# Performance work log

Hardware: AMD Instinct MI355X
Metric: run time of the kernel (lower is better)

Reference implementation:

```python
import jax, jax.numpy as jnp
import numpy as np

B, N, NPOINT, NSAMPLE = 16, 4096, 1024, 32
RADIUS = 0.4
MLP = [64, 64, 128]
IN_CH = 6
EPS = 1e-5


def setup_inputs() -> dict:
    key = jax.random.key(0)
    ks = jax.random.split(key, 2 + 2 * len(MLP))
    inp = {
        "xyz": jax.random.normal(ks[0], (B, 3, N), jnp.float32),
        "points": jax.random.normal(ks[1], (B, 3, N), jnp.float32),
    }
    c_in = IN_CH
    for i, c_out in enumerate(MLP):
        inp[f"W{i}"] = jax.random.normal(ks[2 + 2 * i], (c_out, c_in), jnp.float32) / np.sqrt(c_in).astype(np.float32)
        inp[f"b{i}"] = jnp.zeros((c_out,), jnp.float32)
        inp[f"g{i}"] = jnp.ones((c_out,), jnp.float32)
        inp[f"beta{i}"] = jnp.zeros((c_out,), jnp.float32)
        c_in = c_out
    return inp


def _gather(points, idx):
    # points: [B, N, C], idx: [B, ...] int -> [B, ..., C]
    Bv = points.shape[0]
    flat = idx.reshape(Bv, -1)
    out = jnp.take_along_axis(points, flat[..., None], axis=1)
    return out.reshape(idx.shape + (points.shape[-1],))


def _fps(xyz, npoint):
    # xyz: [B, N, 3] -> centroid indices [B, npoint]
    Bv, Nv, _ = xyz.shape
    bidx = jnp.arange(Bv)

    def step(carry, _):
        dist, far = carry
        cen = xyz[bidx, far][:, None, :]                 # [B,1,3]
        d = jnp.sum((xyz - cen) ** 2, axis=-1)           # [B,N]
        dist = jnp.minimum(dist, d)
        return (dist, jnp.argmax(dist, axis=-1)), far

    init = (jnp.full((Bv, Nv), 1e10, xyz.dtype), jnp.zeros((Bv,), jnp.int32))
    _, cents = jax.lax.scan(step, init, None, length=npoint)
    return jnp.transpose(cents)                          # [B, npoint]


def _square_distance(src, dst):
    # src [B,S,3], dst [B,N,3] -> [B,S,N]
    return (jnp.sum(src ** 2, -1)[:, :, None]
            + jnp.sum(dst ** 2, -1)[:, None, :]
            - 2.0 * jnp.einsum('bsc,bnc->bsn', src, dst))


def _ball_query(radius, nsample, xyz, new_xyz):
    Nv = xyz.shape[1]
    sqr = _square_distance(new_xyz, xyz)                 # [B,S,N]
    arange = jnp.arange(Nv, dtype=jnp.int32)[None, None, :]
    idx = jnp.where(sqr > radius ** 2, Nv, arange)       # invalid -> sentinel N
    idx = jnp.sort(idx, axis=-1)[:, :, :nsample]         # [B,S,K]
    first = idx[:, :, :1]
    return jnp.where(idx == Nv, first, idx)


def reference(xyz, points, W0, b0, g0, beta0, W1, b1, g1, beta1, W2, b2, g2, beta2):
    xyz_t = jnp.transpose(xyz, (0, 2, 1))                # [B,N,3]
    pts_t = jnp.transpose(points, (0, 2, 1))             # [B,N,D]

    fps_idx = _fps(xyz_t, NPOINT)                        # [B,S]
    new_xyz = _gather(xyz_t, fps_idx)                    # [B,S,3]
    idx = _ball_query(RADIUS, NSAMPLE, xyz_t, new_xyz)   # [B,S,K]

    g_xyz = _gather(xyz_t, idx) - new_xyz[:, :, None, :] # [B,S,K,3]
    g_pts = _gather(pts_t, idx)                          # [B,S,K,D]
    feats = jnp.concatenate([g_xyz, g_pts], axis=-1)     # [B,S,K,C]

    for W, b, g, be in ((W0, b0, g0, beta0), (W1, b1, g1, beta1), (W2, b2, g2, beta2)):
        feats = jnp.einsum('bskc,oc->bsko', feats, W) + b
        mean = feats.mean(axis=(0, 1, 2))                # BN train mode stats
        var = feats.var(axis=(0, 1, 2))
        feats = g * (feats - mean) * jax.lax.rsqrt(var + EPS) + be
        feats = jax.nn.relu(feats)

    out = feats.max(axis=2)                              # max over nsample -> [B,S,C]
    return jnp.transpose(new_xyz, (0, 2, 1)), jnp.transpose(out, (0, 2, 1))
```

## Files before the change

### kernel.cpp

```cpp
#include <hip/hip_runtime.h>
#include <hip/hip_bf16.h>

#define B_ 16
#define N_ 4096
#define S_ 1024
#define K_ 32
#define R_ (B_*S_*K_)
#define NBLK_ (R_/64)

typedef unsigned short u16;
typedef __attribute__((ext_vector_type(8))) short bf16x8;
typedef __attribute__((ext_vector_type(4))) float f32x4;

__device__ __forceinline__ u16 f2bf(float f) {
    __hip_bfloat16 h = __float2bfloat16(f);
    return __builtin_bit_cast(u16, h);
}
__device__ __forceinline__ float bf2f(u16 u) {
    unsigned x = ((unsigned)u) << 16;
    return __builtin_bit_cast(float, x);
}

template <int CTRL>
__device__ __forceinline__ double dpp_max_f64(double v) {
    unsigned long long b = (unsigned long long)__double_as_longlong(v);
    int lo = (int)(unsigned)b;
    int hi = (int)(unsigned)(b >> 32);
    int olo = __builtin_amdgcn_update_dpp(lo, lo, CTRL, 0xF, 0xF, false);
    int ohi = __builtin_amdgcn_update_dpp(hi, hi, CTRL, 0xF, 0xF, false);
    double o = __longlong_as_double(
        (long long)(((unsigned long long)(unsigned)ohi << 32) | (unsigned)olo));
    return fmax(v, o);
}

__device__ __forceinline__ double packd(double d, int idx) {
    unsigned long long b = (unsigned long long)__double_as_longlong(d);
    b = (b & ~0xFFFull) | (unsigned)idx;
    return __longlong_as_double((long long)b);
}

__global__ __launch_bounds__(512, 2) void fps_kernel(const float* __restrict__ xyz,
                                                     float* __restrict__ out0) {
    const int b = blockIdx.x;
    const int tid = threadIdx.x;
    const int lane = tid & 63, wid = tid >> 6;
    __shared__ float4 p4[N_];
    __shared__ double candd[2][8];
    const float* xb = xyz + (size_t)b * 3 * N_;

    double x64[8], y64[8], z64[8], q64[8], dist[8];
#pragma unroll
    for (int j = 0; j < 8; ++j) {
        int i = tid + j * 512;
        float x = xb[i], y = xb[N_ + i], z = xb[2 * N_ + i];
        p4[i] = make_float4(x, y, z, 0.f);
        x64[j] = (double)x; y64[j] = (double)y; z64[j] = (double)z;
        q64[j] = x64[j] * x64[j] + y64[j] * y64[j] + z64[j] * z64[j];
        dist[j] = 1e30;
    }
    __syncthreads();

    int far = 0;
    int f0 = 0, f1 = 0;
    for (int s = 0; s < 1023; ++s) {
        float4 c = p4[far];
        f0 = (tid == s) ? far : f0;
        f1 = (tid + 512 == s) ? far : f1;
        double cx = (double)c.x, cy = (double)c.y, cz = (double)c.z;
        double c2p = cx * cx + cy * cy + cz * cz + 1.0;
        double A = -2.0 * cx, Bc = -2.0 * cy, Cc = -2.0 * cz;
#pragma unroll
        for (int j = 0; j < 8; ++j) {
            double d = fma(A, x64[j], fma(Bc, y64[j], fma(Cc, z64[j], q64[j] + c2p)));
            dist[j] = fmin(dist[j], packd(d, tid | (j << 9)));
        }
        double k = fmax(fmax(fmax(dist[0], dist[1]), fmax(dist[2], dist[3])),
                        fmax(fmax(dist[4], dist[5]), fmax(dist[6], dist[7])));
        k = dpp_max_f64<0x111>(k);
        k = dpp_max_f64<0x112>(k);
        k = dpp_max_f64<0x114>(k);
        k = dpp_max_f64<0x118>(k);
        k = dpp_max_f64<0x142>(k);
        k = dpp_max_f64<0x143>(k);
        int buf = s & 1;
        if (lane == 63) candd[buf][wid] = k;
        __syncthreads();
        double k2 = candd[buf][lane & 7];
        k2 = dpp_max_f64<0xB1>(k2);
        k2 = dpp_max_f64<0x4E>(k2);
        k2 = dpp_max_f64<0x124>(k2);
        unsigned lo = (unsigned)(unsigned long long)__double_as_longlong(k2);
        far = (int)(__builtin_amdgcn_readfirstlane(lo) & 0xFFFu);
    }
    if (tid == 511) f1 = far;
    {
        float4 c0 = p4[f0];
        out0[(size_t)b * 3072 + tid]        = c0.x;
        out0[(size_t)b * 3072 + 1024 + tid] = c0.y;
        out0[(size_t)b * 3072 + 2048 + tid] = c0.z;
        float4 c1 = p4[f1];
        out0[(size_t)b * 3072 + 512 + tid]        = c1.x;
        out0[(size_t)b * 3072 + 1024 + 512 + tid] = c1.y;
        out0[(size_t)b * 3072 + 2048 + 512 + tid] = c1.z;
    }
}

__global__ __launch_bounds__(256) void prep_kernel(const float* __restrict__ xyz,
                                                   const float* __restrict__ W1,
                                                   const float* __restrict__ W2,
                                                   u16* __restrict__ W1bf,
                                                   u16* __restrict__ W2bf,
                                                   double4* __restrict__ xyzq) {
    int t = blockIdx.x * 256 + threadIdx.x;
    if (t < 4096) W1bf[t] = f2bf(W1[t]);
    if (t < 8192) W2bf[t] = f2bf(W2[t]);
    int b = t >> 12, i = t & 4095;
    const float* xb = xyz + (size_t)b * 3 * N_;
    double x = (double)xb[i], y = (double)xb[N_ + i], z = (double)xb[2 * N_ + i];
    double4 v; v.x = x; v.y = y; v.z = z; v.w = x * x + y * y + z * z;
    xyzq[t] = v;
}

__global__ __launch_bounds__(256) void ballq_kernel(const double4* __restrict__ xyzq,
                                                    const float* __restrict__ out0,
                                                    int* __restrict__ idxbuf) {
    int wid = threadIdx.x >> 6, lane = threadIdx.x & 63;
    int m = blockIdx.x * 4 + wid;
    int b = m >> 10, s = m & 1023;
    const double4* pb = xyzq + (size_t)b * N_;
    double cx = (double)out0[b * 3072 + s];
    double cy = (double)out0[b * 3072 + 1024 + s];
    double cz = (double)out0[b * 3072 + 2048 + s];
    double c2 = cx * cx + cy * cy + cz * cz;
    const double rr = 0.4 * 0.4;
    int* ob = idxbuf + (size_t)m * K_;
    int cnt = 0, first = -1;
    for (int ch = 0; ch < N_ / 64; ++ch) {
        int i = ch * 64 + lane;
        double4 p = pb[i];
        double dot = cx * p.x + cy * p.y + cz * p.z;
        double sqr = (c2 + p.w) - 2.0 * dot;
        bool in = !(sqr > rr);
        unsigned long long mask = __ballot(in);
        if (in) {
            int pos = cnt + __popcll(mask & ((1ull << lane) - 1ull));
            if (pos < K_) ob[pos] = i;
        }
        if (cnt == 0 && mask) first = ch * 64 + (__ffsll((long long)mask) - 1);
        cnt += __popcll(mask);
        if (cnt >= K_) break;
    }
    if (cnt < K_ && lane >= cnt && lane < K_) ob[lane] = first;
}

__global__ __launch_bounds__(256) void gather_stats0(
        const float* __restrict__ xyz, const float* __restrict__ pts,
        const float* __restrict__ out0, const int* __restrict__ idxbuf,
        const float* __restrict__ W0, const float* __restrict__ b0,
        float* __restrict__ F, float2* __restrict__ part) {
    __shared__ float Fs[64][6];
    __shared__ float W0s[384];
    __shared__ float b0s[64];
    __shared__ float2 red[4][64];
    int tid = threadIdx.x;
    long rowbase = (long)blockIdx.x * 64;
    for (int e = tid; e < 384; e += 256) {
        int r = e / 6, c = e - r * 6;
        long rw = rowbase + r;
        int b = (int)(rw >> 15);
        int s = ((int)(rw & 32767)) >> 5;
        int i = idxbuf[rw];
        float v;
        if (c < 3)
            v = xyz[(size_t)b * 3 * N_ + c * N_ + i] - out0[b * 3072 + c * 1024 + s];
        else
            v = pts[(size_t)b * 3 * N_ + (c - 3) * N_ + i];
        Fs[r][c] = v;
        F[rw * 6 + c] = v;
    }
    if (tid < 64) b0s[tid] = b0[tid];
    for (int t = tid; t < 384; t += 256) W0s[t] = W0[t];
    __syncthreads();
    int o = tid & 63, rg = tid >> 6;
    float w[6];
#pragma unroll
    for (int c = 0; c < 6; ++c) w[c] = W0s[o * 6 + c];
    float sum = 0.f, sq = 0.f;
#pragma unroll
    for (int rr = 0; rr < 16; ++rr) {
        int rl = rg * 16 + rr;
        float y = b0s[o];
#pragma unroll
        for (int c = 0; c < 6; ++c) y += Fs[rl][c] * w[c];
        sum += y; sq += y * y;
    }
    red[rg][o] = make_float2(sum, sq);
    __syncthreads();
    if (tid < 64) {
        float2 t0 = red[0][tid], t1 = red[1][tid], t2 = red[2][tid], t3 = red[3][tid];
        part[(size_t)blockIdx.x * 64 + tid] =
            make_float2(t0.x + t1.x + t2.x + t3.x, t0.y + t1.y + t2.y + t3.y);
    }
}

__global__ __launch_bounds__(256) void reduce_stats(const float2* __restrict__ part,
                                                    int nblk, int C,
                                                    const float* __restrict__ g,
                                                    const float* __restrict__ beta,
                                                    float* __restrict__ scale,
                                                    float* __restrict__ shift) {
    int o = blockIdx.x;
    int tid = threadIdx.x;
    double s = 0.0, q = 0.0;
    for (int i = tid; i < nblk; i += 256) {
        float2 v = part[(size_t)i * C + o];
        s += (double)v.x; q += (double)v.y;
    }
    __shared__ double ss[256], qq[256];
    ss[tid] = s; qq[tid] = q;
    __syncthreads();
    for (int m = 128; m > 0; m >>= 1) {
        if (tid < m) { ss[tid] += ss[tid + m]; qq[tid] += qq[tid + m]; }
        __syncthreads();
    }
    if (tid == 0) {
        const double Rd = (double)R_;
        double mean = ss[0] / Rd;
        double var = qq[0] / Rd - mean * mean;
        double sc = (double)g[o] / sqrt(var + 1e-5);
        scale[o] = (float)sc;
        shift[o] = (float)((double)beta[o] - mean * sc);
    }
}

__global__ __launch_bounds__(256) void layer1_mfma(
        const float* __restrict__ F, const float* __restrict__ W0,
        const float* __restrict__ b0, const float* __restrict__ scale0,
        const float* __restrict__ shift0, const u16* __restrict__ W1bf,
        const float* __restrict__ b1, u16* __restrict__ Y1bf,
        float2* __restrict__ part) {
    __shared__ float Fs[64][6];
    __shared__ float W0s[384];
    __shared__ float b0s[64], sc0[64], sh0[64];
    __shared__ u16 Xs[64][72];
    __shared__ float ssum[16][64];
    __shared__ float ssq[16][64];
    int tid = threadIdx.x;
    long rowbase = (long)blockIdx.x * 64;
    for (int t = tid; t < 384; t += 256) { Fs[t / 6][t % 6] = F[rowbase * 6 + t]; W0s[t] = W0[t]; }
    if (tid < 64) { b0s[tid] = b0[tid]; sc0[tid] = scale0[tid]; sh0[tid] = shift0[tid]; }
    __syncthreads();
    {
        int o = tid & 63, rg = tid >> 6;
        float w[6];
#pragma unroll
        for (int c = 0; c < 6; ++c) w[c] = W0s[o * 6 + c];
        float sc = sc0[o], sh = sh0[o], bb = b0s[o];
#pragma unroll
        for (int rr = 0; rr < 16; ++rr) {
            int rl = rg * 16 + rr;
            float y = bb;
#pragma unroll
            for (int c = 0; c < 6; ++c) y += Fs[rl][c] * w[c];
            Xs[rl][o] = f2bf(fmaxf(sc * y + sh, 0.f));
        }
    }
    __syncthreads();
    int l = tid & 63, w = tid >> 6;
    int ar = l & 15, kg = l >> 4;
    bf16x8 a0 = *(const bf16x8*)&Xs[w * 16 + ar][kg * 8];
    bf16x8 a1 = *(const bf16x8*)&Xs[w * 16 + ar][32 + kg * 8];
    f32x4 acc[4];
#pragma unroll
    for (int t4 = 0; t4 < 4; ++t4) acc[t4] = (f32x4){0.f, 0.f, 0.f, 0.f};
#pragma unroll
    for (int t4 = 0; t4 < 4; ++t4) {
        const u16* wp = &W1bf[(t4 * 16 + ar) * 64 + kg * 8];
        bf16x8 bfr0 = *(const bf16x8*)wp;
        bf16x8 bfr1 = *(const bf16x8*)(wp + 32);
        acc[t4] = __builtin_amdgcn_mfma_f32_16x16x32_bf16(a0, bfr0, acc[t4], 0, 0, 0);
        acc[t4] = __builtin_amdgcn_mfma_f32_16x16x32_bf16(a1, bfr1, acc[t4], 0, 0, 0);
    }
#pragma unroll
    for (int t4 = 0; t4 < 4; ++t4) {
        int col = t4 * 16 + ar;
        float bb = b1[col];
        float s = 0.f, q = 0.f;
#pragma unroll
        for (int r = 0; r < 4; ++r) {
            float y = acc[t4][r] + bb;
            int row = w * 16 + kg * 4 + r;
            Y1bf[(rowbase + row) * 64 + col] = f2bf(y);
            s += y; q += y * y;
        }
        ssum[w * 4 + kg][col] = s;
        ssq[w * 4 + kg][col] = q;
    }
    __syncthreads();
    if (tid < 64) {
        float s = 0.f, q = 0.f;
#pragma unroll
        for (int i = 0; i < 16; ++i) { s += ssum[i][tid]; q += ssq[i][tid]; }
        part[(size_t)blockIdx.x * 64 + tid] = make_float2(s, q);
    }
}

__global__ __launch_bounds__(256) void layer2_mfma(
        const u16* __restrict__ Y1bf, const float* __restrict__ scale1,
        const float* __restrict__ shift1, const u16* __restrict__ W2bf,
        const float* __restrict__ b2, float* __restrict__ gmax,
        float* __restrict__ gmin, float2* __restrict__ part) {
    __shared__ u16 Xs[64][72];
    __shared__ float sc1s[64], sh1s[64];
    __shared__ float mxs[16][128], mns[16][128];
    __shared__ float ssum[16][128], ssq[16][128];
    int tid = threadIdx.x;
    long rowbase = (long)blockIdx.x * 64;
    if (tid < 64) { sc1s[tid] = scale1[tid]; sh1s[tid] = shift1[tid]; }
    __syncthreads();
    {
        int r = tid >> 2, seg = (tid & 3) * 16;
        const u16* yp = &Y1bf[(rowbase + r) * 64 + seg];
        bf16x8 v0 = *(const bf16x8*)yp;
        bf16x8 v1 = *(const bf16x8*)(yp + 8);
#pragma unroll
        for (int j = 0; j < 8; ++j) {
            float x0 = fmaxf(sc1s[seg + j] * bf2f((u16)v0[j]) + sh1s[seg + j], 0.f);
            float x1 = fmaxf(sc1s[seg + 8 + j] * bf2f((u16)v1[j]) + sh1s[seg + 8 + j], 0.f);
            Xs[r][seg + j] = f2bf(x0);
            Xs[r][seg + 8 + j] = f2bf(x1);
        }
    }
    __syncthreads();
    int l = tid & 63, w = tid >> 6;
    int ar = l & 15, kg = l >> 4;
    bf16x8 a0 = *(const bf16x8*)&Xs[w * 16 + ar][kg * 8];
    bf16x8 a1 = *(const bf16x8*)&Xs[w * 16 + ar][32 + kg * 8];
    f32x4 acc[8];
#pragma unroll
    for (int t8 = 0; t8 < 8; ++t8) acc[t8] = (f32x4){0.f, 0.f, 0.f, 0.f};
#pragma unroll
    for (int t8 = 0; t8 < 8; ++t8) {
        const u16* wp = &W2bf[(t8 * 16 + ar) * 64 + kg * 8];
        bf16x8 bfr0 = *(const bf16x8*)wp;
        bf16x8 bfr1 = *(const bf16x8*)(wp + 32);
        acc[t8] = __builtin_amdgcn_mfma_f32_16x16x32_bf16(a0, bfr0, acc[t8], 0, 0, 0);
        acc[t8] = __builtin_amdgcn_mfma_f32_16x16x32_bf16(a1, bfr1, acc[t8], 0, 0, 0);
    }
#pragma unroll
    for (int t8 = 0; t8 < 8; ++t8) {
        int col = t8 * 16 + ar;
        float bb = b2[col];
        float y0 = acc[t8][0] + bb, y1 = acc[t8][1] + bb;
        float y2 = acc[t8][2] + bb, y3 = acc[t8][3] + bb;
        ssum[w * 4 + kg][col] = y0 + y1 + y2 + y3;
        ssq[w * 4 + kg][col] = y0 * y0 + y1 * y1 + y2 * y2 + y3 * y3;
        mxs[w * 4 + kg][col] = fmaxf(fmaxf(y0, y1), fmaxf(y2, y3));
        mns[w * 4 + kg][col] = fminf(fminf(y0, y1), fminf(y2, y3));
    }
    __syncthreads();
    if (tid < 128) {
        int col = tid;
        float s = 0.f, q = 0.f;
        float m0 = -3.0e38f, m1 = -3.0e38f, n0 = 3.0e38f, n1 = 3.0e38f;
#pragma unroll
        for (int i = 0; i < 8; ++i) {
            s += ssum[i][col]; q += ssq[i][col];
            m0 = fmaxf(m0, mxs[i][col]); n0 = fminf(n0, mns[i][col]);
        }
#pragma unroll
        for (int i = 8; i < 16; ++i) {
            s += ssum[i][col]; q += ssq[i][col];
            m1 = fmaxf(m1, mxs[i][col]); n1 = fminf(n1, mns[i][col]);
        }
        part[(size_t)blockIdx.x * 128 + col] = make_float2(s, q);
        gmax[((size_t)blockIdx.x * 2 + 0) * 128 + col] = m0;
        gmax[((size_t)blockIdx.x * 2 + 1) * 128 + col] = m1;
        gmin[((size_t)blockIdx.x * 2 + 0) * 128 + col] = n0;
        gmin[((size_t)blockIdx.x * 2 + 1) * 128 + col] = n1;
    }
}

__global__ __launch_bounds__(256) void final_kernel(const float* __restrict__ gmax,
                                                    const float* __restrict__ gmin,
                                                    const float* __restrict__ scale2,
                                                    const float* __restrict__ shift2,
                                                    float* __restrict__ out1) {
    int b = blockIdx.x, st = blockIdx.y, ot = blockIdx.z;
    __shared__ float tile[32][33];
    int tid = threadIdx.x;
    for (int e = tid; e < 1024; e += 256) {
        int sl = e >> 5, ol = e & 31;
        int s = st * 32 + sl, o = ot * 32 + ol;
        size_t m = (size_t)b * 1024 + s;
        float sc = scale2[o];
        float v = (sc >= 0.f) ? gmax[m * 128 + o] : gmin[m * 128 + o];
        tile[sl][ol] = fmaxf(sc * v + shift2[o], 0.f);
    }
    __syncthreads();
    for (int e = tid; e < 1024; e += 256) {
        int ol = e >> 5, sl = e & 31;
        int s = st * 32 + sl, o = ot * 32 + ol;
        out1[(size_t)b * 131072 + (size_t)o * 1024 + s] = tile[sl][ol];
    }
}

extern "C" void kernel_launch(void* const* d_in, const int* in_sizes, int n_in,
                              void* d_out, int out_size, void* d_ws, size_t ws_size,
                              hipStream_t stream) {
    const float* xyz   = (const float*)d_in[0];
    const float* pts   = (const float*)d_in[1];
    const float* W0    = (const float*)d_in[2];
    const float* b0    = (const float*)d_in[3];
    const float* g0    = (const float*)d_in[4];
    const float* beta0 = (const float*)d_in[5];
    const float* W1    = (const float*)d_in[6];
    const float* b1    = (const float*)d_in[7];
    const float* g1    = (const float*)d_in[8];
    const float* beta1 = (const float*)d_in[9];
    const float* W2    = (const float*)d_in[10];
    const float* b2    = (const float*)d_in[11];
    const float* g2    = (const float*)d_in[12];
    const float* beta2 = (const float*)d_in[13];

    float* out0 = (float*)d_out;
    float* out1 = (float*)d_out + 49152;

    char* w = (char*)d_ws;
    size_t off = 0;
    double4* xyzq = (double4*)(w + off);  off += (size_t)B_ * N_ * 32;
    int*    idxbuf = (int*)(w + off);    off += (size_t)R_ * 4;
    float*  F      = (float*)(w + off);  off += (size_t)R_ * 6 * 4;
    u16*    Y1bf   = (u16*)(w + off);    off += (size_t)R_ * 64 * 2;
    float*  gmax   = (float*)(w + off);  off += (size_t)B_ * S_ * 128 * 4;
    float*  gmin   = (float*)(w + off);  off += (size_t)B_ * S_ * 128 * 4;
    float2* part   = (float2*)(w + off); off += (size_t)NBLK_ * 128 * 2 * 4;
    u16*    W1bf   = (u16*)(w + off);    off += 4096 * 2;
    u16*    W2bf   = (u16*)(w + off);    off += 8192 * 2;
    float*  ss     = (float*)(w + off);  off += 512 * 4;
    float* scale0 = ss,       *shift0 = ss + 64;
    float* scale1 = ss + 128, *shift1 = ss + 192;
    float* scale2 = ss + 256, *shift2 = ss + 384;

    prep_kernel<<<256, 256, 0, stream>>>(xyz, W1, W2, W1bf, W2bf, xyzq);
    fps_kernel<<<B_, 512, 0, stream>>>(xyz, out0);
    ballq_kernel<<<(B_ * S_) / 4, 256, 0, stream>>>(xyzq, out0, idxbuf);
    gather_stats0<<<NBLK_, 256, 0, stream>>>(xyz, pts, out0, idxbuf, W0, b0, F, part);
    reduce_stats<<<64, 256, 0, stream>>>(part, NBLK_, 64, g0, beta0, scale0, shift0);
    layer1_mfma<<<NBLK_, 256, 0, stream>>>(F, W0, b0, scale0, shift0, W1bf, b1, Y1bf, part);
    reduce_stats<<<64, 256, 0, stream>>>(part, NBLK_, 64, g1, beta1, scale1, shift1);
    layer2_mfma<<<NBLK_, 256, 0, stream>>>(Y1bf, scale1, shift1, W2bf, b2, gmax, gmin, part);
    reduce_stats<<<128, 256, 0, stream>>>(part, NBLK_, 128, g2, beta2, scale2, shift2);
    final_kernel<<<dim3(B_, 32, 4), 256, 0, stream>>>(gmax, gmin, scale2, shift2, out1);
}
```

Measured before the change: 864.5 us.

## Fuse gather into ball query and derive layer-0 BN stats from input moments

The ball-query kernel now also gathers the grouped features and writes F. It accumulates the 6 first moments and 21 second moments of the inputs per block. Layer-0 batch-norm mean and variance come analytically from these moments and W0/b0 in double precision, which removes the separate gather_stats0 pass and the 64-channel reduction. The FPS kernel also caches precomputed -2x and |x|^2+1 doubles in shared memory to drop per-step centroid arithmetic, at the cost of more LDS and one block per CU. The moment-based variance is more prone to cancellation, and the per-block moments are summed in fp32.

```diff
diff --git a/kernel.cpp b/kernel.cpp
--- a/kernel.cpp
+++ b/kernel.cpp
@@ -39,12 +39,12 @@
     return __longlong_as_double((long long)b);
 }
 
-__global__ __launch_bounds__(512, 2) void fps_kernel(const float* __restrict__ xyz,
+__global__ __launch_bounds__(512, 1) void fps_kernel(const float* __restrict__ xyz,
                                                      float* __restrict__ out0) {
     const int b = blockIdx.x;
     const int tid = threadIdx.x;
     const int lane = tid & 63, wid = tid >> 6;
-    __shared__ float4 p4[N_];
+    __shared__ double4 cd[N_];
     __shared__ double candd[2][8];
     const float* xb = xyz + (size_t)b * 3 * N_;
 
@@ -53,9 +53,11 @@
     for (int j = 0; j < 8; ++j) {
         int i = tid + j * 512;
         float x = xb[i], y = xb[N_ + i], z = xb[2 * N_ + i];
-        p4[i] = make_float4(x, y, z, 0.f);
-        x64[j] = (double)x; y64[j] = (double)y; z64[j] = (double)z;
-        q64[j] = x64[j] * x64[j] + y64[j] * y64[j] + z64[j] * z64[j];
+        double dx = (double)x, dy = (double)y, dz = (double)z;
+        double q = dx * dx + dy * dy + dz * dz;
+        double4 v; v.x = -2.0 * dx; v.y = -2.0 * dy; v.z = -2.0 * dz; v.w = q + 1.0;
+        cd[i] = v;
+        x64[j] = dx; y64[j] = dy; z64[j] = dz; q64[j] = q;
         dist[j] = 1e30;
     }
     __syncthreads();
@@ -63,15 +65,12 @@
     int far = 0;
     int f0 = 0, f1 = 0;
     for (int s = 0; s < 1023; ++s) {
-        float4 c = p4[far];
+        double4 C = cd[far];
         f0 = (tid == s) ? far : f0;
         f1 = (tid + 512 == s) ? far : f1;
-        double cx = (double)c.x, cy = (double)c.y, cz = (double)c.z;
-        double c2p = cx * cx + cy * cy + cz * cz + 1.0;
-        double A = -2.0 * cx, Bc = -2.0 * cy, Cc = -2.0 * cz;
 #pragma unroll
         for (int j = 0; j < 8; ++j) {
-            double d = fma(A, x64[j], fma(Bc, y64[j], fma(Cc, z64[j], q64[j] + c2p)));
+            double d = fma(C.x, x64[j], fma(C.y, y64[j], fma(C.z, z64[j], q64[j] + C.w)));
             dist[j] = fmin(dist[j], packd(d, tid | (j << 9)));
         }
         double k = fmax(fmax(fmax(dist[0], dist[1]), fmax(dist[2], dist[3])),
@@ -94,14 +93,14 @@
     }
     if (tid == 511) f1 = far;
     {
-        float4 c0 = p4[f0];
-        out0[(size_t)b * 3072 + tid]        = c0.x;
-        out0[(size_t)b * 3072 + 1024 + tid] = c0.y;
-        out0[(size_t)b * 3072 + 2048 + tid] = c0.z;
-        float4 c1 = p4[f1];
-        out0[(size_t)b * 3072 + 512 + tid]        = c1.x;
-        out0[(size_t)b * 3072 + 1024 + 512 + tid] = c1.y;
-        out0[(size_t)b * 3072 + 2048 + 512 + tid] = c1.z;
+        double4 c0 = cd[f0];
+        out0[(size_t)b * 3072 + tid]        = (float)(-0.5 * c0.x);
+        out0[(size_t)b * 3072 + 1024 + tid] = (float)(-0.5 * c0.y);
+        out0[(size_t)b * 3072 + 2048 + tid] = (float)(-0.5 * c0.z);
+        double4 c1 = cd[f1];
+        out0[(size_t)b * 3072 + 512 + tid]        = (float)(-0.5 * c1.x);
+        out0[(size_t)b * 3072 + 1024 + 512 + tid] = (float)(-0.5 * c1.y);
+        out0[(size_t)b * 3072 + 2048 + 512 + tid] = (float)(-0.5 * c1.z);
     }
 }
 
@@ -121,9 +120,14 @@
     xyzq[t] = v;
 }
 
-__global__ __launch_bounds__(256) void ballq_kernel(const double4* __restrict__ xyzq,
-                                                    const float* __restrict__ out0,
-                                                    int* __restrict__ idxbuf) {
+__global__ __launch_bounds__(256) void ballq_gather(
+        const double4* __restrict__ xyzq, const float* __restrict__ out0,
+        const float* __restrict__ xyz, const float* __restrict__ pts,
+        int* __restrict__ idxbuf, float* __restrict__ F,
+        float* __restrict__ part0) {
+    __shared__ int idxs[4][32];
+    __shared__ float Ftile[128][6];
+    __shared__ float red[8][27];
     int wid = threadIdx.x >> 6, lane = threadIdx.x & 63;
     int m = blockIdx.x * 4 + wid;
     int b = m >> 10, s = m & 1023;
@@ -144,63 +148,99 @@
         unsigned long long mask = __ballot(in);
         if (in) {
             int pos = cnt + __popcll(mask & ((1ull << lane) - 1ull));
-            if (pos < K_) ob[pos] = i;
+            if (pos < K_) { ob[pos] = i; idxs[wid][pos] = i; }
         }
         if (cnt == 0 && mask) first = ch * 64 + (__ffsll((long long)mask) - 1);
         cnt += __popcll(mask);
         if (cnt >= K_) break;
     }
-    if (cnt < K_ && lane >= cnt && lane < K_) ob[lane] = first;
-}
-
-__global__ __launch_bounds__(256) void gather_stats0(
-        const float* __restrict__ xyz, const float* __restrict__ pts,
-        const float* __restrict__ out0, const int* __restrict__ idxbuf,
-        const float* __restrict__ W0, const float* __restrict__ b0,
-        float* __restrict__ F, float2* __restrict__ part) {
-    __shared__ float Fs[64][6];
-    __shared__ float W0s[384];
-    __shared__ float b0s[64];
-    __shared__ float2 red[4][64];
+    if (cnt < K_ && lane >= cnt && lane < K_) { ob[lane] = first; idxs[wid][lane] = first; }
+    __syncthreads();
+    if (lane < 32) {
+        int i = idxs[wid][lane];
+        int rl = wid * 32 + lane;
+        long rw = (long)m * 32 + lane;
+        float cxf = out0[b * 3072 + s], cyf = out0[b * 3072 + 1024 + s], czf = out0[b * 3072 + 2048 + s];
+        const float* xb = xyz + (size_t)b * 3 * N_;
+        const float* pp = pts + (size_t)b * 3 * N_;
+        float f0v = xb[i] - cxf, f1v = xb[N_ + i] - cyf, f2v = xb[2 * N_ + i] - czf;
+        float f3v = pp[i], f4v = pp[N_ + i], f5v = pp[2 * N_ + i];
+        Ftile[rl][0] = f0v; Ftile[rl][1] = f1v; Ftile[rl][2] = f2v;
+        Ftile[rl][3] = f3v; Ftile[rl][4] = f4v; Ftile[rl][5] = f5v;
+        float* Fg = F + rw * 6;
+        Fg[0] = f0v; Fg[1] = f1v; Fg[2] = f2v; Fg[3] = f3v; Fg[4] = f4v; Fg[5] = f5v;
+    }
+    __syncthreads();
+    int t = threadIdx.x;
+    if (t < 216) {
+        const int c1t[27] = {0,1,2,3,4,5, 0,0,0,0,0,0, 1,1,1,1,1, 2,2,2,2, 3,3,3, 4,4, 5};
+        const int c2t[27] = {0,1,2,3,4,5, 0,1,2,3,4,5, 1,2,3,4,5, 2,3,4,5, 3,4,5, 4,5, 5};
+        int st = t % 27, g = t / 27;
+        float acc = 0.f;
+        if (st < 6) {
+            for (int r = g * 16; r < g * 16 + 16; ++r) acc += Ftile[r][st];
+        } else {
+            int a = c1t[st], c = c2t[st];
+            for (int r = g * 16; r < g * 16 + 16; ++r) acc += Ftile[r][a] * Ftile[r][c];
+        }
+        red[g][st] = acc;
+    }
+    __syncthreads();
+    if (t < 27) {
+        float a = 0.f;
+#pragma unroll
+        for (int g = 0; g < 8; ++g) a += red[g][t];
+        part0[(size_t)blockIdx.x * 27 + t] = a;
+    }
+}
+
+__global__ __launch_bounds__(256) void reduce27(const float* __restrict__ part0,
+                                                double* __restrict__ G) {
+    int st = blockIdx.x;
     int tid = threadIdx.x;
-    long rowbase = (long)blockIdx.x * 64;
-    for (int e = tid; e < 384; e += 256) {
-        int r = e / 6, c = e - r * 6;
-        long rw = rowbase + r;
-        int b = (int)(rw >> 15);
-        int s = ((int)(rw & 32767)) >> 5;
-        int i = idxbuf[rw];
-        float v;
-        if (c < 3)
-            v = xyz[(size_t)b * 3 * N_ + c * N_ + i] - out0[b * 3072 + c * 1024 + s];
-        else
-            v = pts[(size_t)b * 3 * N_ + (c - 3) * N_ + i];
-        Fs[r][c] = v;
-        F[rw * 6 + c] = v;
-    }
-    if (tid < 64) b0s[tid] = b0[tid];
-    for (int t = tid; t < 384; t += 256) W0s[t] = W0[t];
-    __syncthreads();
-    int o = tid & 63, rg = tid >> 6;
-    float w[6];
-#pragma unroll
-    for (int c = 0; c < 6; ++c) w[c] = W0s[o * 6 + c];
-    float sum = 0.f, sq = 0.f;
-#pragma unroll
-    for (int rr = 0; rr < 16; ++rr) {
-        int rl = rg * 16 + rr;
-        float y = b0s[o];
-#pragma unroll
-        for (int c = 0; c < 6; ++c) y += Fs[rl][c] * w[c];
-        sum += y; sq += y * y;
-    }
-    red[rg][o] = make_float2(sum, sq);
-    __syncthreads();
-    if (tid < 64) {
-        float2 t0 = red[0][tid], t1 = red[1][tid], t2 = red[2][tid], t3 = red[3][tid];
-        part[(size_t)blockIdx.x * 64 + tid] =
-            make_float2(t0.x + t1.x + t2.x + t3.x, t0.y + t1.y + t2.y + t3.y);
-    }
+    double s = 0.0;
+    for (int i = tid; i < 4096; i += 256) s += (double)part0[(size_t)i * 27 + st];
+    __shared__ double ss[256];
+    ss[tid] = s;
+    __syncthreads();
+    for (int m = 128; m > 0; m >>= 1) {
+        if (tid < m) ss[tid] += ss[tid + m];
+        __syncthreads();
+    }
+    if (tid == 0) G[st] = ss[0];
+}
+
+__global__ __launch_bounds__(64) void stats0_final(const double* __restrict__ G,
+                                                   const float* __restrict__ W0,
+                                                   const float* __restrict__ b0,
+                                                   const float* __restrict__ g0,
+                                                   const float* __restrict__ beta0,
+                                                   float* __restrict__ scale0,
+                                                   float* __restrict__ shift0) {
+    int o = threadIdx.x;
+    double w[6], mvec[6];
+#pragma unroll
+    for (int c = 0; c < 6; ++c) { w[c] = (double)W0[o * 6 + c]; mvec[c] = G[c]; }
+    double dot = 0.0;
+#pragma unroll
+    for (int c = 0; c < 6; ++c) dot += w[c] * mvec[c];
+    const double Rd = (double)R_;
+    double bb = (double)b0[o];
+    double mu = dot / Rd + bb;
+    double quad = 0.0;
+    int k = 6;
+#pragma unroll
+    for (int a = 0; a < 6; ++a)
+#pragma unroll
+        for (int c = a; c < 6; ++c) {
+            double g = G[k++];
+            quad += (a == c) ? w[a] * w[c] * g : 2.0 * w[a] * w[c] * g;
+        }
+    double ey2 = (quad + 2.0 * bb * dot) / Rd + bb * bb;
+    double var = ey2 - mu * mu;
+    double sc = (double)g0[o] / sqrt(var + 1e-5);
+    scale0[o] = (float)sc;
+    shift0[o] = (float)((double)beta0[o] - mu * sc);
 }
 
 __global__ __launch_bounds__(256) void reduce_stats(const float2* __restrict__ part,
@@ -435,6 +475,8 @@
     float*  gmax   = (float*)(w + off);  off += (size_t)B_ * S_ * 128 * 4;
     float*  gmin   = (float*)(w + off);  off += (size_t)B_ * S_ * 128 * 4;
     float2* part   = (float2*)(w + off); off += (size_t)NBLK_ * 128 * 2 * 4;
+    float*  part0  = (float*)(w + off);  off += (size_t)4096 * 27 * 4;
+    double* G27    = (double*)(w + off); off += 32 * 8;
     u16*    W1bf   = (u16*)(w + off);    off += 4096 * 2;
     u16*    W2bf   = (u16*)(w + off);    off += 8192 * 2;
     float*  ss     = (float*)(w + off);  off += 512 * 4;
@@ -444,9 +486,9 @@
 
     prep_kernel<<<256, 256, 0, stream>>>(xyz, W1, W2, W1bf, W2bf, xyzq);
     fps_kernel<<<B_, 512, 0, stream>>>(xyz, out0);
-    ballq_kernel<<<(B_ * S_) / 4, 256, 0, stream>>>(xyzq, out0, idxbuf);
-    gather_stats0<<<NBLK_, 256, 0, stream>>>(xyz, pts, out0, idxbuf, W0, b0, F, part);
-    reduce_stats<<<64, 256, 0, stream>>>(part, NBLK_, 64, g0, beta0, scale0, shift0);
+    ballq_gather<<<(B_ * S_) / 4, 256, 0, stream>>>(xyzq, out0, xyz, pts, idxbuf, F, part0);
+    reduce27<<<27, 256, 0, stream>>>(part0, G27);
+    stats0_final<<<1, 64, 0, stream>>>(G27, W0, b0, g0, beta0, scale0, shift0);
     layer1_mfma<<<NBLK_, 256, 0, stream>>>(F, W0, b0, scale0, shift0, W1bf, b1, Y1bf, part);
     reduce_stats<<<64, 256, 0, stream>>>(part, NBLK_, 64, g1, beta1, scale1, shift1);
     layer2_mfma<<<NBLK_, 256, 0, stream>>>(Y1bf, scale1, shift1, W2bf, b2, gmax, gmin, part);
```

After: 813.7 us. -5.9%, faster.
